# Performance work log

Measured on AMD Instinct MI355X. Metric: run time of the kernel, lower is better.

## Reference

```python
import jax, jax.numpy as jnp
import numpy as np

L, B, D, H = 512, 128, 512, 512

def setup_inputs() -> dict:
    key = jax.random.key(0)
    ks = jax.random.split(key, 6)
    s = 1.0 / np.sqrt(H)
    return {
        "x": jax.random.normal(ks[0], (L, B, D), dtype=jnp.float32),
        "h": jax.random.normal(ks[1], (B, H), dtype=jnp.float32),
        "Wx_w": jax.random.normal(ks[2], (H, D), dtype=jnp.float32) * s,
        "Wx_b": jax.random.normal(ks[3], (H,), dtype=jnp.float32) * s,
        "Wh_w": jax.random.normal(ks[4], (H, H), dtype=jnp.float32) * s,
        "Wh_b": jax.random.normal(ks[5], (H,), dtype=jnp.float32) * s,
    }

def reference(x, h, Wx_w, Wx_b, Wh_w, Wh_b):
    # Precompute input projection for all timesteps in one big GEMM:
    # Wx(x_t) + bx + bh  -> [L, B, H]
    xproj = jnp.einsum('lbd,hd->lbh', x, Wx_w) + Wx_b + Wh_b

    def step(h, xp_t):
        # h_t = tanh(Wx(x_t) + Wh(h_{t-1}))
        h_new = jnp.tanh(xp_t + h @ Wh_w.T)
        return h_new, h_new

    h_last, hAll = jax.lax.scan(step, h, xproj)
    return hAll, h_last
```

## Files before the change

### kernel.cpp

```cpp
#include <hip/hip_runtime.h>
#include <math.h>

#define Lt 512
#define Bn 128
#define Dd 512
#define Hh 512
#define BH (Bn * Hh)

typedef __attribute__((ext_vector_type(4))) float f32x4;
typedef __attribute__((ext_vector_type(8))) __bf16 bf16x8;
typedef __attribute__((ext_vector_type(8))) unsigned short u16x8;
typedef __attribute__((ext_vector_type(4))) unsigned int u32x4;

#define MFMA16 __builtin_amdgcn_mfma_f32_16x16x32_bf16

__device__ __forceinline__ float bf2f(unsigned short s) {
    return __uint_as_float(((unsigned)s) << 16);
}
__device__ __forceinline__ unsigned short f2bf_rne(float f) {
    unsigned u = __float_as_uint(f);
    u = (u + 0x7FFFu + ((u >> 16) & 1u)) >> 16;
    return (unsigned short)u;
}
__device__ __forceinline__ float tanh_fast(float z) {
    float e = __expf(2.f * z);
    return 1.f - 2.f * __builtin_amdgcn_rcpf(e + 1.f);
}
__device__ __forceinline__ unsigned pack_hi16(unsigned a, unsigned b) {
    return __builtin_amdgcn_perm(b, a, 0x07060302u);
}
__device__ __forceinline__ unsigned pack_lo16(unsigned a, unsigned b) {
    return __builtin_amdgcn_perm(b, a, 0x05040100u);
}

__global__ void zero_flags_kernel(unsigned* __restrict__ flags) {
    int i = blockIdx.x * 256 + threadIdx.x;
    if (i < 256) flags[i] = 0;
}

__device__ __forceinline__ void stage_wslice(const float* __restrict__ W, int j0g,
                                             int stride, unsigned short* hiA,
                                             unsigned short* loA, int lane) {
    #pragma unroll 4
    for (int it = 0; it < 32; ++it) {
        int idx = (it * 64 + lane) * 4;
        int j = idx >> 9;
        int k = idx & 511;
        float4 w = *(const float4*)(W + (size_t)(j0g + j) * stride + k);
        int base = j * 520 + k;
        unsigned short s0 = f2bf_rne(w.x); hiA[base + 0] = s0; loA[base + 0] = f2bf_rne(w.x - bf2f(s0));
        unsigned short s1 = f2bf_rne(w.y); hiA[base + 1] = s1; loA[base + 1] = f2bf_rne(w.y - bf2f(s1));
        unsigned short s2 = f2bf_rne(w.z); hiA[base + 2] = s2; loA[base + 2] = f2bf_rne(w.z - bf2f(s2));
        unsigned short s3 = f2bf_rne(w.w); hiA[base + 3] = s3; loA[base + 3] = f2bf_rne(w.w - bf2f(s3));
    }
}

__global__ __launch_bounds__(64, 1) void rnn_fused_kernel(
    const float* __restrict__ x, const float* __restrict__ h0in,
    const float* __restrict__ Wx, const float* __restrict__ bx,
    const float* __restrict__ Wh, const float* __restrict__ bh,
    float* __restrict__ out, unsigned* __restrict__ hpk, unsigned* flags) {

    __shared__ unsigned short WxHi[16 * 520], WxLo[16 * 520];
    __shared__ unsigned short WhHi[16 * 520], WhLo[16 * 520];

    const int lane = threadIdx.x;
    const int bg = blockIdx.x & 7;
    const int jg = blockIdx.x >> 3;
    const int b0g = bg * 16;
    const int j0g = jg * 16;

    stage_wslice(Wx, j0g, Dd, WxHi, WxLo, lane);
    stage_wslice(Wh, j0g, Hh, WhHi, WhLo, lane);
    __syncthreads();

    const int rw = lane & 15;
    const int quad = lane >> 4;
    const unsigned short* WxHiR = WxHi + rw * 520;
    const unsigned short* WxLoR = WxLo + rw * 520;
    const unsigned short* WhHiR = WhHi + rw * 520;
    const unsigned short* WhLoR = WhLo + rw * 520;
    const float bsum = bx[j0g + rw] + bh[j0g + rw];

    #pragma unroll
    for (int r = 0; r < 4; ++r) {
        int b = b0g + quad * 4 + r;
        float v = h0in[(size_t)b * Hh + (j0g + rw)];
        unsigned u = __float_as_uint(v);
        unsigned hb = u >> 16;
        unsigned lb = __float_as_uint(v - __uint_as_float(u & 0xFFFF0000u)) >> 16;
        __hip_atomic_store(hpk + BH + (size_t)b * Hh + (j0g + rw),
                           (hb << 16) | lb, __ATOMIC_RELAXED,
                           __HIP_MEMORY_SCOPE_AGENT);
    }
    asm volatile("s_waitcnt vmcnt(0)" ::: "memory");
    if (lane == 0) {
        __hip_atomic_store(&flags[bg * 32 + jg], 1u, __ATOMIC_RELAXED,
                           __HIP_MEMORY_SCOPE_AGENT);
    }

    for (int t = 0; t < Lt; ++t) {
        f32x4 aHH = {0.f, 0.f, 0.f, 0.f};
        f32x4 aHL = {0.f, 0.f, 0.f, 0.f};
        f32x4 aLH = {0.f, 0.f, 0.f, 0.f};

        const float* xrow = x + ((size_t)t * Bn + (b0g + rw)) * Dd;
        #pragma unroll
        for (int c = 0; c < 16; ++c) {
            int kk = c * 32 + quad * 8;
            float4 v0 = *(const float4*)(xrow + kk);
            float4 v1 = *(const float4*)(xrow + kk + 4);
            unsigned u0 = __float_as_uint(v0.x), u1 = __float_as_uint(v0.y);
            unsigned u2 = __float_as_uint(v0.z), u3 = __float_as_uint(v0.w);
            unsigned u4 = __float_as_uint(v1.x), u5 = __float_as_uint(v1.y);
            unsigned u6 = __float_as_uint(v1.z), u7 = __float_as_uint(v1.w);
            u32x4 hi4 = {pack_hi16(u0, u1), pack_hi16(u2, u3),
                         pack_hi16(u4, u5), pack_hi16(u6, u7)};
            float l0 = v0.x - __uint_as_float(u0 & 0xFFFF0000u);
            float l1 = v0.y - __uint_as_float(u1 & 0xFFFF0000u);
            float l2 = v0.z - __uint_as_float(u2 & 0xFFFF0000u);
            float l3 = v0.w - __uint_as_float(u3 & 0xFFFF0000u);
            float l4 = v1.x - __uint_as_float(u4 & 0xFFFF0000u);
            float l5 = v1.y - __uint_as_float(u5 & 0xFFFF0000u);
            float l6 = v1.z - __uint_as_float(u6 & 0xFFFF0000u);
            float l7 = v1.w - __uint_as_float(u7 & 0xFFFF0000u);
            u32x4 lo4 = {pack_hi16(__float_as_uint(l0), __float_as_uint(l1)),
                         pack_hi16(__float_as_uint(l2), __float_as_uint(l3)),
                         pack_hi16(__float_as_uint(l4), __float_as_uint(l5)),
                         pack_hi16(__float_as_uint(l6), __float_as_uint(l7))};
            bf16x8 aH = __builtin_bit_cast(bf16x8, hi4);
            bf16x8 aL = __builtin_bit_cast(bf16x8, lo4);
            bf16x8 bH = __builtin_bit_cast(bf16x8, *(const u16x8*)(WxHiR + kk));
            bf16x8 bL = __builtin_bit_cast(bf16x8, *(const u16x8*)(WxLoR + kk));
            aHH = MFMA16(aH, bH, aHH, 0, 0, 0);
            aHL = MFMA16(aH, bL, aHL, 0, 0, 0);
            aLH = MFMA16(aL, bH, aLH, 0, 0, 0);
        }

        {
            const unsigned tgt = (unsigned)t + 1u;
            while (true) {
                unsigned v = __hip_atomic_load(&flags[bg * 32 + (lane & 31)],
                                               __ATOMIC_RELAXED,
                                               __HIP_MEMORY_SCOPE_AGENT);
                if (__ballot(v >= tgt) == 0xFFFFFFFFFFFFFFFFull) break;
            }
        }

        const unsigned* hrow =
            hpk + (size_t)((t + 1) & 1) * BH + (size_t)(b0g + rw) * Hh;
        #pragma unroll
        for (int c = 0; c < 16; ++c) {
            int kk = c * 32 + quad * 8;
            unsigned long long p0 = __hip_atomic_load(
                (const unsigned long long*)(hrow + kk + 0),
                __ATOMIC_RELAXED, __HIP_MEMORY_SCOPE_AGENT);
            unsigned long long p1 = __hip_atomic_load(
                (const unsigned long long*)(hrow + kk + 2),
                __ATOMIC_RELAXED, __HIP_MEMORY_SCOPE_AGENT);
            unsigned long long p2 = __hip_atomic_load(
                (const unsigned long long*)(hrow + kk + 4),
                __ATOMIC_RELAXED, __HIP_MEMORY_SCOPE_AGENT);
            unsigned long long p3 = __hip_atomic_load(
                (const unsigned long long*)(hrow + kk + 6),
                __ATOMIC_RELAXED, __HIP_MEMORY_SCOPE_AGENT);
            unsigned q0 = (unsigned)p0, q1 = (unsigned)(p0 >> 32);
            unsigned q2 = (unsigned)p1, q3 = (unsigned)(p1 >> 32);
            unsigned q4 = (unsigned)p2, q5 = (unsigned)(p2 >> 32);
            unsigned q6 = (unsigned)p3, q7 = (unsigned)(p3 >> 32);
            u32x4 hi4 = {pack_hi16(q0, q1), pack_hi16(q2, q3),
                         pack_hi16(q4, q5), pack_hi16(q6, q7)};
            u32x4 lo4 = {pack_lo16(q0, q1), pack_lo16(q2, q3),
                         pack_lo16(q4, q5), pack_lo16(q6, q7)};
            bf16x8 aH = __builtin_bit_cast(bf16x8, hi4);
            bf16x8 aL = __builtin_bit_cast(bf16x8, lo4);
            bf16x8 bH = __builtin_bit_cast(bf16x8, *(const u16x8*)(WhHiR + kk));
            bf16x8 bL = __builtin_bit_cast(bf16x8, *(const u16x8*)(WhLoR + kk));
            aHH = MFMA16(aH, bH, aHH, 0, 0, 0);
            aHL = MFMA16(aH, bL, aHL, 0, 0, 0);
            aLH = MFMA16(aL, bH, aLH, 0, 0, 0);
        }

        f32x4 acc = aHH + aHL + aLH;

        float hv[4];
        #pragma unroll
        for (int r = 0; r < 4; ++r) hv[r] = tanh_fast(acc[r] + bsum);

        unsigned* hw = hpk + (size_t)(t & 1) * BH;
        #pragma unroll
        for (int r = 0; r < 4; ++r) {
            int b = b0g + quad * 4 + r;
            unsigned u = __float_as_uint(hv[r]);
            unsigned hb = u >> 16;
            unsigned lb =
                __float_as_uint(hv[r] - __uint_as_float(u & 0xFFFF0000u)) >> 16;
            __hip_atomic_store(hw + (size_t)b * Hh + (j0g + rw), (hb << 16) | lb,
                               __ATOMIC_RELAXED, __HIP_MEMORY_SCOPE_AGENT);
        }
        asm volatile("s_waitcnt vmcnt(0)" ::: "memory");
        if (lane == 0 && t + 1 < Lt) {
            __hip_atomic_store(&flags[bg * 32 + jg], (unsigned)(t + 2),
                               __ATOMIC_RELAXED, __HIP_MEMORY_SCOPE_AGENT);
        }

        #pragma unroll
        for (int r = 0; r < 4; ++r) {
            int b = b0g + quad * 4 + r;
            out[((size_t)t * Bn + b) * Hh + (j0g + rw)] = hv[r];
        }
        if (t == Lt - 1) {
            #pragma unroll
            for (int r = 0; r < 4; ++r) {
                int b = b0g + quad * 4 + r;
                out[(size_t)Lt * BH + (size_t)b * Hh + (j0g + rw)] = hv[r];
            }
        }
    }
}

extern "C" void kernel_launch(void* const* d_in, const int* in_sizes, int n_in,
                              void* d_out, int out_size, void* d_ws, size_t ws_size,
                              hipStream_t stream) {
    const float* x    = (const float*)d_in[0];
    const float* h0   = (const float*)d_in[1];
    const float* Wx_w = (const float*)d_in[2];
    const float* Wx_b = (const float*)d_in[3];
    const float* Wh_w = (const float*)d_in[4];
    const float* Wh_b = (const float*)d_in[5];
    float* out = (float*)d_out;

    unsigned* hpk   = (unsigned*)d_ws;
    unsigned* flags = hpk + 2 * BH;

    zero_flags_kernel<<<1, 256, 0, stream>>>(flags);
    rnn_fused_kernel<<<256, 64, 0, stream>>>(x, h0, Wx_w, Wx_b, Wh_w, Wh_b,
                                             out, hpk, flags);
}
```

Measured before the change: 3.068 ms.

## Split input projection into a separate parallel GEMM kernel before recurrence

```diff
diff --git a/kernel.cpp b/kernel.cpp
--- a/kernel.cpp
+++ b/kernel.cpp
@@ -55,56 +55,36 @@
     }
 }
 
-__global__ __launch_bounds__(64, 1) void rnn_fused_kernel(
-    const float* __restrict__ x, const float* __restrict__ h0in,
-    const float* __restrict__ Wx, const float* __restrict__ bx,
-    const float* __restrict__ Wh, const float* __restrict__ bh,
-    float* __restrict__ out, unsigned* __restrict__ hpk, unsigned* flags) {
-
-    __shared__ unsigned short WxHi[16 * 520], WxLo[16 * 520];
-    __shared__ unsigned short WhHi[16 * 520], WhLo[16 * 520];
+__global__ __launch_bounds__(64, 1) void xproj_kernel(
+    const float* __restrict__ x, const float* __restrict__ Wx,
+    const float* __restrict__ bx, const float* __restrict__ bh,
+    float* __restrict__ out) {
+
+    __shared__ unsigned short WHi[16 * 520], WLo[16 * 520];
 
     const int lane = threadIdx.x;
-    const int bg = blockIdx.x & 7;
-    const int jg = blockIdx.x >> 3;
-    const int b0g = bg * 16;
-    const int j0g = jg * 16;
-
-    stage_wslice(Wx, j0g, Dd, WxHi, WxLo, lane);
-    stage_wslice(Wh, j0g, Hh, WhHi, WhLo, lane);
+    const int cls  = blockIdx.x & 7;
+    const int idx  = blockIdx.x >> 3;
+    const int jg   = idx & 31;
+    const int slab = cls * 8 + (idx >> 5);
+    const int j0g  = jg * 16;
+
+    stage_wslice(Wx, j0g, Dd, WHi, WLo, lane);
     __syncthreads();
 
     const int rw = lane & 15;
     const int quad = lane >> 4;
-    const unsigned short* WxHiR = WxHi + rw * 520;
-    const unsigned short* WxLoR = WxLo + rw * 520;
-    const unsigned short* WhHiR = WhHi + rw * 520;
-    const unsigned short* WhLoR = WhLo + rw * 520;
+    const unsigned short* HiR = WHi + rw * 520;
+    const unsigned short* LoR = WLo + rw * 520;
     const float bsum = bx[j0g + rw] + bh[j0g + rw];
-
-    #pragma unroll
-    for (int r = 0; r < 4; ++r) {
-        int b = b0g + quad * 4 + r;
-        float v = h0in[(size_t)b * Hh + (j0g + rw)];
-        unsigned u = __float_as_uint(v);
-        unsigned hb = u >> 16;
-        unsigned lb = __float_as_uint(v - __uint_as_float(u & 0xFFFF0000u)) >> 16;
-        __hip_atomic_store(hpk + BH + (size_t)b * Hh + (j0g + rw),
-                           (hb << 16) | lb, __ATOMIC_RELAXED,
-                           __HIP_MEMORY_SCOPE_AGENT);
-    }
-    asm volatile("s_waitcnt vmcnt(0)" ::: "memory");
-    if (lane == 0) {
-        __hip_atomic_store(&flags[bg * 32 + jg], 1u, __ATOMIC_RELAXED,
-                           __HIP_MEMORY_SCOPE_AGENT);
-    }
-
-    for (int t = 0; t < Lt; ++t) {
+    const int row0 = slab * 1024;
+
+    for (int rt = 0; rt < 64; ++rt) {
+        const int r0 = row0 + rt * 16;
         f32x4 aHH = {0.f, 0.f, 0.f, 0.f};
         f32x4 aHL = {0.f, 0.f, 0.f, 0.f};
         f32x4 aLH = {0.f, 0.f, 0.f, 0.f};
-
-        const float* xrow = x + ((size_t)t * Bn + (b0g + rw)) * Dd;
+        const float* xrow = x + (size_t)(r0 + rw) * Dd;
         #pragma unroll
         for (int c = 0; c < 16; ++c) {
             int kk = c * 32 + quad * 8;
@@ -130,11 +110,65 @@
                          pack_hi16(__float_as_uint(l6), __float_as_uint(l7))};
             bf16x8 aH = __builtin_bit_cast(bf16x8, hi4);
             bf16x8 aL = __builtin_bit_cast(bf16x8, lo4);
-            bf16x8 bH = __builtin_bit_cast(bf16x8, *(const u16x8*)(WxHiR + kk));
-            bf16x8 bL = __builtin_bit_cast(bf16x8, *(const u16x8*)(WxLoR + kk));
+            bf16x8 bH = __builtin_bit_cast(bf16x8, *(const u16x8*)(HiR + kk));
+            bf16x8 bL = __builtin_bit_cast(bf16x8, *(const u16x8*)(LoR + kk));
             aHH = MFMA16(aH, bH, aHH, 0, 0, 0);
             aHL = MFMA16(aH, bL, aHL, 0, 0, 0);
             aLH = MFMA16(aL, bH, aLH, 0, 0, 0);
+        }
+        f32x4 acc = aHH + aHL + aLH;
+        #pragma unroll
+        for (int r = 0; r < 4; ++r) {
+            int m = r0 + quad * 4 + r;
+            out[(size_t)m * Hh + (j0g + rw)] = acc[r] + bsum;
+        }
+    }
+}
+
+__global__ __launch_bounds__(64, 1) void rnn_rec_kernel(
+    const float* __restrict__ h0in, const float* __restrict__ Wh,
+    float* __restrict__ out, unsigned* __restrict__ hpk, unsigned* flags) {
+
+    __shared__ unsigned short WhHi[16 * 520], WhLo[16 * 520];
+
+    const int lane = threadIdx.x;
+    const int bg = blockIdx.x & 7;
+    const int jg = blockIdx.x >> 3;
+    const int b0g = bg * 16;
+    const int j0g = jg * 16;
+
+    stage_wslice(Wh, j0g, Hh, WhHi, WhLo, lane);
+    __syncthreads();
+
+    const int rw = lane & 15;
+    const int quad = lane >> 4;
+    const unsigned short* WhHiR = WhHi + rw * 520;
+    const unsigned short* WhLoR = WhLo + rw * 520;
+
+    #pragma unroll
+    for (int r = 0; r < 4; ++r) {
+        int b = b0g + quad * 4 + r;
+        float v = h0in[(size_t)b * Hh + (j0g + rw)];
+        unsigned u = __float_as_uint(v);
+        unsigned hb = u >> 16;
+        unsigned lb = __float_as_uint(v - __uint_as_float(u & 0xFFFF0000u)) >> 16;
+        __hip_atomic_store(hpk + BH + (size_t)b * Hh + (j0g + rw),
+                           (hb << 16) | lb, __ATOMIC_RELAXED,
+                           __HIP_MEMORY_SCOPE_AGENT);
+    }
+    asm volatile("s_waitcnt vmcnt(0)" ::: "memory");
+    if (lane == 0) {
+        __hip_atomic_store(&flags[bg * 32 + jg], 1u, __ATOMIC_RELAXED,
+                           __HIP_MEMORY_SCOPE_AGENT);
+    }
+
+    for (int t = 0; t < Lt; ++t) {
+        float xpv[4];
+        {
+            const float* xprow = out + (size_t)t * BH;
+            #pragma unroll
+            for (int r = 0; r < 4; ++r)
+                xpv[r] = xprow[(size_t)(b0g + quad * 4 + r) * Hh + (j0g + rw)];
         }
 
         {
@@ -147,6 +181,9 @@
             }
         }
 
+        f32x4 aHH = {0.f, 0.f, 0.f, 0.f};
+        f32x4 aHL = {0.f, 0.f, 0.f, 0.f};
+        f32x4 aLH = {0.f, 0.f, 0.f, 0.f};
         const unsigned* hrow =
             hpk + (size_t)((t + 1) & 1) * BH + (size_t)(b0g + rw) * Hh;
         #pragma unroll
@@ -185,7 +222,7 @@
 
         float hv[4];
         #pragma unroll
-        for (int r = 0; r < 4; ++r) hv[r] = tanh_fast(acc[r] + bsum);
+        for (int r = 0; r < 4; ++r) hv[r] = tanh_fast(acc[r] + xpv[r]);
 
         unsigned* hw = hpk + (size_t)(t & 1) * BH;
         #pragma unroll
@@ -234,6 +271,6 @@
     unsigned* flags = hpk + 2 * BH;
 
     zero_flags_kernel<<<1, 256, 0, stream>>>(flags);
-    rnn_fused_kernel<<<256, 64, 0, stream>>>(x, h0, Wx_w, Wx_b, Wh_w, Wh_b,
-                                             out, hpk, flags);
-}
+    xproj_kernel<<<2048, 64, 0, stream>>>(x, Wx_w, Wx_b, Wh_b, out);
+    rnn_rec_kernel<<<256, 64, 0, stream>>>(h0, Wh_w, out, hpk, flags);
+}
```

Result: slower. 3.272 ms (+6.6%).
